# Kernel optimization log

Measured on AMD Instinct MI355X. Metric: run time of the kernel, lower is better.

Reference implementation:

```python
import jax, jax.numpy as jnp
import numpy as np

N_NODES, N_EDGES, B, K, D = 200000, 500000, 8192, 32, 128
E_DIM, E_EMB, N_CLASS = 128, 128, 60


def setup_inputs() -> dict:
    key = jax.random.key(0)
    ks = jax.random.split(key, 16)
    s = lambda k, shape, scale=0.05: jax.random.normal(k, shape, dtype=jnp.float32) * scale
    return {
        'memory_emb': s(ks[0], (N_NODES, D), 1.0),
        'edge_feat': s(ks[1], (N_EDGES, E_DIM), 1.0),
        'W_q': s(ks[2], (D, D)),
        'W_k': s(ks[3], (D, D)),
        'a': s(ks[4], (2 * D,)),
        'We_w': s(ks[5], (E_DIM, E_EMB)),
        'We_b': s(ks[6], (E_EMB,)),
        'Wuc': s(ks[7], (D + 2 * D + E_EMB, D)),
        'Wc1': s(ks[8], (D, 128)),
        'Wc2': s(ks[9], (128, N_CLASS)),
        'src_idxs': jax.random.randint(ks[10], (B,), 0, N_NODES),
        'dst_idxs': jax.random.randint(ks[11], (B,), 0, N_NODES),
        'edge_idxs': jax.random.randint(ks[12], (B,), 0, N_EDGES),
        'src_neighbors': jax.random.randint(ks[13], (B, K), 0, N_NODES),
        'dst_neighbors': jax.random.randint(ks[14], (B, K), 0, N_NODES),
    }


def reference(memory_emb, edge_feat, W_q, W_k, a, We_w, We_b, Wuc, Wc1, Wc2,
              src_idxs, dst_idxs, edge_idxs, src_neighbors, dst_neighbors):
    def attend(idxs, nbrs):
        self_emb = memory_emb[idxs]                      # [B, D] gather
        nb = memory_emb[nbrs]                            # [B, K, D] gather
        q = self_emb @ W_q                               # [B, D]
        k = jnp.einsum('bkd,de->bke', nb, W_k)           # [B, K, D]
        # GAT-style score: leaky_relu(a . [q || k])
        sq = q @ a[:D]                                   # [B]
        sk = jnp.einsum('bkd,d->bk', k, a[D:])           # [B, K]
        score = jax.nn.leaky_relu(sq[:, None] + sk, 0.2)
        attn = jax.nn.softmax(score, axis=-1)            # [B, K]
        agg = jnp.einsum('bk,bkd->bd', attn, k)          # [B, D]
        return self_emb, agg

    src_e, src_h = attend(src_idxs, src_neighbors)
    dst_e, dst_h = attend(dst_idxs, dst_neighbors)
    e = edge_feat[edge_idxs] @ We_w + We_b               # edge embedding [B, E_EMB]
    msg_src = jax.nn.relu(jnp.concatenate([src_e, src_h, dst_h, e], -1) @ Wuc)
    msg_dst = jax.nn.relu(jnp.concatenate([dst_e, dst_h, src_h, e], -1) @ Wuc)
    logits_src = jax.nn.relu(msg_src @ Wc1) @ Wc2
    logits_dst = jax.nn.relu(msg_dst @ Wc1) @ Wc2
    return jnp.stack([logits_src, logits_dst])           # [2, B, N_CLASS]
```

## Files before the change

kernel.cpp:

```cpp
#include <hip/hip_runtime.h>

#define D 128
#define KNBR 32
#define BATCH 8192
#define NCLASS 60
#define NB 16
#define NP 32

__global__ __launch_bounds__(256) void k_prep(
    const float* __restrict__ Wq, const float* __restrict__ Wk,
    const float* __restrict__ a, const float* __restrict__ Wew,
    const float* __restrict__ Web, const float* __restrict__ Wuc,
    float* __restrict__ wqa, float* __restrict__ wka,
    float* __restrict__ be, float* __restrict__ Wcomb2)
{
    __shared__ float sB[128][129];
    int blk = blockIdx.x, tid = threadIdx.x;
    if (blk == 0) {
        for (int t = tid; t < 128 * 128; t += 256) sB[t >> 7][t & 127] = Wq[t];
        __syncthreads();
        if (tid < 128) {
            float s = 0.f;
            for (int j = 0; j < D; ++j) s += sB[tid][j] * a[j];
            wqa[tid] = s;
        }
        __syncthreads();
        for (int t = tid; t < 128 * 128; t += 256) sB[t >> 7][t & 127] = Wk[t];
        __syncthreads();
        if (tid < 128) {
            float s = 0.f;
            for (int j = 0; j < D; ++j) s += sB[tid][j] * a[D + j];
            wka[tid] = s;
        }
    } else if (blk == 1) {
        if (tid < 128) {
            float acc = 0.f;
            for (int j = 0; j < D; ++j) acc += Web[j] * Wuc[(size_t)(384 + j) * D + tid];
            be[tid] = acc;
        }
    } else {
        int g  = (blk - 2) >> 4;
        int rb = ((blk - 2) & 15) * 8;
        const float* A = (g == 2) ? Wew : Wk;
        const float* B = Wuc + (size_t)(128 + g * 128) * D;
        for (int t = tid; t < 128 * 128; t += 256) sB[t >> 7][t & 127] = B[t];
        __syncthreads();
        int j = tid & 127, half = tid >> 7;
        float acc[4] = {0.f, 0.f, 0.f, 0.f};
        int r0 = rb + half * 4;
        for (int t = 0; t < 128; ++t) {
            float bv = sB[t][j];
            #pragma unroll
            for (int m = 0; m < 4; ++m)
                acc[m] = fmaf(A[(size_t)(r0 + m) * D + t], bv, acc[m]);
        }
        #pragma unroll
        for (int m = 0; m < 4; ++m)
            Wcomb2[(size_t)(g * 128 + r0 + m) * D + j] = acc[m];
    }
}

__global__ __launch_bounds__(256, 2) void k_fused(
    const float* __restrict__ mem, const float* __restrict__ edge_feat,
    const float* __restrict__ Wuc, const float* __restrict__ Wcomb2,
    const float* __restrict__ be,
    const float* __restrict__ wqa, const float* __restrict__ wka,
    const float* __restrict__ Wc1, const float* __restrict__ Wc2,
    const int* __restrict__ src_idxs, const int* __restrict__ dst_idxs,
    const int* __restrict__ edge_idxs,
    const int* __restrict__ src_nb, const int* __restrict__ dst_nb,
    float* __restrict__ out)
{
    __shared__ __align__(16) float s_self[NP * 132];
    __shared__ __align__(16) float s_nbsum[NP * 132];
    __shared__ __align__(16) float Ast[32 * 33];
    __shared__ __align__(16) float Ws[32 * 128];
    __shared__ __align__(16) float msgT[128 * 35];
    __shared__ int s_eidx[NB];

    int tid = threadIdx.x;
    int b0 = blockIdx.x * NB;
    int lane = tid & 31;
    int grp  = tid >> 5;

    if (tid < NB) s_eidx[tid] = edge_idxs[b0 + tid];

    float4 wq4 = ((const float4*)wqa)[lane];
    float4 wk4 = ((const float4*)wka)[lane];

    for (int it = 0; it < 4; ++it) {
        int p = it * 8 + grp;
        int side = p >> 4;
        int bb = b0 + (p & 15);
        int self_idx = (side ? dst_idxs : src_idxs)[bb];
        int nb_idx = (side ? dst_nb : src_nb)[(size_t)bb * KNBR + lane];

        float4 sv = ((const float4*)(mem + (size_t)self_idx * D))[lane];
        *(float4*)&s_self[p * 132 + lane * 4] = sv;
        float sp = sv.x * wq4.x + sv.y * wq4.y + sv.z * wq4.z + sv.w * wq4.w;
        #pragma unroll
        for (int m = 1; m <= 16; m <<= 1) sp += __shfl_xor(sp, m, 32);
        float sq = sp;

        float myscore = 0.f;
        #pragma unroll 4
        for (int k = 0; k < KNBR; ++k) {
            int ik = __shfl(nb_idx, k, 32);
            float4 v = ((const float4*)(mem + (size_t)ik * D))[lane];
            float pr = v.x * wk4.x + v.y * wk4.y + v.z * wk4.z + v.w * wk4.w;
            #pragma unroll
            for (int m = 1; m <= 16; m <<= 1) pr += __shfl_xor(pr, m, 32);
            if (k == lane) myscore = pr;
        }
        float x = sq + myscore;
        x = (x >= 0.f) ? x : 0.2f * x;
        float mx = x;
        #pragma unroll
        for (int m = 1; m <= 16; m <<= 1) mx = fmaxf(mx, __shfl_xor(mx, m, 32));
        float e = __expf(x - mx);
        float sum = e;
        #pragma unroll
        for (int m = 1; m <= 16; m <<= 1) sum += __shfl_xor(sum, m, 32);
        float attn = e / sum;

        float4 acc = make_float4(0.f, 0.f, 0.f, 0.f);
        #pragma unroll 4
        for (int k = 0; k < KNBR; ++k) {
            int ik = __shfl(nb_idx, k, 32);
            float ak = __shfl(attn, k, 32);
            float4 v = ((const float4*)(mem + (size_t)ik * D))[lane];
            acc.x = fmaf(ak, v.x, acc.x);
            acc.y = fmaf(ak, v.y, acc.y);
            acc.z = fmaf(ak, v.z, acc.z);
            acc.w = fmaf(ak, v.w, acc.w);
        }
        *(float4*)&s_nbsum[p * 132 + lane * 4] = acc;
    }
    __syncthreads();

    int tr = tid >> 4, tc = tid & 15;
    int lc = tid & 31, lr = tid >> 5;
    int wc = tid & 127, wk2 = tid >> 7;
    float accB[2][8];
    #pragma unroll
    for (int i = 0; i < 2; ++i)
        #pragma unroll
        for (int j = 0; j < 8; ++j) accB[i][j] = 0.f;

    for (int kt = 0; kt < 16; ++kt) {
        int seg = kt >> 2, off = (kt & 3) * 32;
        #pragma unroll
        for (int q = 0; q < 4; ++q) {
            int r = lr + 8 * q;
            float v;
            if (seg == 0)      v = s_self[r * 132 + off + lc];
            else if (seg == 1) v = s_nbsum[r * 132 + off + lc];
            else if (seg == 2) v = s_nbsum[(r ^ 16) * 132 + off + lc];
            else               v = edge_feat[(size_t)s_eidx[r & 15] * D + off + lc];
            Ast[lc * 33 + r] = v;
        }
        int krow0 = kt * 32;
        #pragma unroll
        for (int pp = 0; pp < 16; ++pp) {
            int kk = wk2 + 2 * pp;
            int gr = krow0 + kk;
            Ws[kk * 128 + wc] = (gr < 128) ? Wuc[(size_t)gr * D + wc]
                                           : Wcomb2[(size_t)(gr - 128) * D + wc];
        }
        __syncthreads();
        #pragma unroll 8
        for (int kk = 0; kk < 32; ++kk) {
            float a0 = Ast[kk * 33 + tr * 2];
            float a1 = Ast[kk * 33 + tr * 2 + 1];
            float4 w0 = *(const float4*)&Ws[kk * 128 + tc * 4];
            float4 w1 = *(const float4*)&Ws[kk * 128 + 64 + tc * 4];
            float wr[8] = {w0.x, w0.y, w0.z, w0.w, w1.x, w1.y, w1.z, w1.w};
            #pragma unroll
            for (int j = 0; j < 8; ++j) {
                accB[0][j] = fmaf(a0, wr[j], accB[0][j]);
                accB[1][j] = fmaf(a1, wr[j], accB[1][j]);
            }
        }
        __syncthreads();
    }
    {
        float4 bv0 = *(const float4*)&be[tc * 4];
        float4 bv1 = *(const float4*)&be[64 + tc * 4];
        float b8[8] = {bv0.x, bv0.y, bv0.z, bv0.w, bv1.x, bv1.y, bv1.z, bv1.w};
        #pragma unroll
        for (int i = 0; i < 2; ++i) {
            int r = tr * 2 + i;
            #pragma unroll
            for (int j = 0; j < 4; ++j) {
                msgT[(tc * 4 + j) * 35 + r]        = fmaxf(accB[i][j] + b8[j], 0.f);
                msgT[(64 + tc * 4 + j) * 35 + r]   = fmaxf(accB[i][j + 4] + b8[j + 4], 0.f);
            }
        }
    }
    __syncthreads();

    float accC[2][8];
    #pragma unroll
    for (int i = 0; i < 2; ++i)
        #pragma unroll
        for (int j = 0; j < 8; ++j) accC[i][j] = 0.f;

    for (int kt = 0; kt < 4; ++kt) {
        int off = kt * 32;
        #pragma unroll
        for (int pp = 0; pp < 16; ++pp) {
            int kk = wk2 + 2 * pp;
            Ws[kk * 128 + wc] = Wc1[(size_t)(off + kk) * D + wc];
        }
        __syncthreads();
        #pragma unroll 8
        for (int kk = 0; kk < 32; ++kk) {
            float a0 = msgT[(off + kk) * 35 + tr * 2];
            float a1 = msgT[(off + kk) * 35 + tr * 2 + 1];
            float4 w0 = *(const float4*)&Ws[kk * 128 + tc * 4];
            float4 w1 = *(const float4*)&Ws[kk * 128 + 64 + tc * 4];
            float wr[8] = {w0.x, w0.y, w0.z, w0.w, w1.x, w1.y, w1.z, w1.w};
            #pragma unroll
            for (int j = 0; j < 8; ++j) {
                accC[0][j] = fmaf(a0, wr[j], accC[0][j]);
                accC[1][j] = fmaf(a1, wr[j], accC[1][j]);
            }
        }
        __syncthreads();
    }
    #pragma unroll
    for (int i = 0; i < 2; ++i) {
        int r = tr * 2 + i;
        #pragma unroll
        for (int j = 0; j < 4; ++j) {
            msgT[(tc * 4 + j) * 35 + r]      = fmaxf(accC[i][j], 0.f);
            msgT[(64 + tc * 4 + j) * 35 + r] = fmaxf(accC[i][j + 4], 0.f);
        }
    }
    __syncthreads();

    int r2 = tid & 31;
    int cs = tid >> 5;
    float acc2[8];
    #pragma unroll
    for (int j = 0; j < 8; ++j) acc2[j] = 0.f;

    for (int kt = 0; kt < 4; ++kt) {
        int off = kt * 32;
        for (int t = tid; t < 32 * 64; t += 256) {
            int kk = t >> 6, c = t & 63;
            Ws[t] = (c < NCLASS) ? Wc2[(size_t)(off + kk) * NCLASS + c] : 0.f;
        }
        __syncthreads();
        #pragma unroll 4
        for (int kk = 0; kk < 32; ++kk) {
            float h = msgT[(off + kk) * 35 + r2];
            float4 w0 = *(const float4*)&Ws[kk * 64 + cs * 8];
            float4 w1 = *(const float4*)&Ws[kk * 64 + cs * 8 + 4];
            acc2[0] = fmaf(h, w0.x, acc2[0]);
            acc2[1] = fmaf(h, w0.y, acc2[1]);
            acc2[2] = fmaf(h, w0.z, acc2[2]);
            acc2[3] = fmaf(h, w0.w, acc2[3]);
            acc2[4] = fmaf(h, w1.x, acc2[4]);
            acc2[5] = fmaf(h, w1.y, acc2[5]);
            acc2[6] = fmaf(h, w1.z, acc2[6]);
            acc2[7] = fmaf(h, w1.w, acc2[7]);
        }
        __syncthreads();
    }
    {
        int side = r2 >> 4;
        int bb = b0 + (r2 & 15);
        size_t orow = ((size_t)side * BATCH + bb) * NCLASS;
        #pragma unroll
        for (int j = 0; j < 8; ++j) {
            int c = cs * 8 + j;
            if (c < NCLASS) out[orow + c] = acc2[j];
        }
    }
}

extern "C" void kernel_launch(void* const* d_in, const int* in_sizes, int n_in,
                              void* d_out, int out_size, void* d_ws, size_t ws_size,
                              hipStream_t stream) {
    const float* mem       = (const float*)d_in[0];
    const float* edge_feat = (const float*)d_in[1];
    const float* Wq        = (const float*)d_in[2];
    const float* Wk        = (const float*)d_in[3];
    const float* a         = (const float*)d_in[4];
    const float* Wew       = (const float*)d_in[5];
    const float* Web       = (const float*)d_in[6];
    const float* Wuc       = (const float*)d_in[7];
    const float* Wc1       = (const float*)d_in[8];
    const float* Wc2       = (const float*)d_in[9];
    const int* src_idxs    = (const int*)d_in[10];
    const int* dst_idxs    = (const int*)d_in[11];
    const int* edge_idxs   = (const int*)d_in[12];
    const int* src_nb      = (const int*)d_in[13];
    const int* dst_nb      = (const int*)d_in[14];
    float* out = (float*)d_out;

    float* ws = (float*)d_ws;
    float* Wcomb2 = ws;
    float* be     = ws + 49152;
    float* wqa    = ws + 49280;
    float* wka    = ws + 49408;

    k_prep<<<50, 256, 0, stream>>>(Wq, Wk, a, Wew, Web, Wuc, wqa, wka, be, Wcomb2);
    k_fused<<<BATCH / NB, 256, 0, stream>>>(mem, edge_feat, Wuc, Wcomb2, be,
                                            wqa, wka, Wc1, Wc2,
                                            src_idxs, dst_idxs, edge_idxs,
                                            src_nb, dst_nb, out);
}
```

Measured before the change: 550.5 us.

## Precompute per-node attention scores to avoid second neighbor gather

Adds a kernel that computes q- and k-score scalars for every node by streaming the embedding table once. The fused kernel then only reads a scalar per neighbor for the softmax, eliminating one of the two full-row neighbor gathers. Shared memory is reorganized (transposed neighbor sums, self rows re-read from global) to allow higher occupancy. It adds a full pass over all nodes regardless of batch usage.

```diff
diff --git a/kernel.cpp b/kernel.cpp
--- a/kernel.cpp
+++ b/kernel.cpp
@@ -60,22 +60,46 @@
     }
 }
 
-__global__ __launch_bounds__(256, 2) void k_fused(
+__global__ __launch_bounds__(256) void k_scores(
+    const float* __restrict__ mem,
+    const float* __restrict__ wqa, const float* __restrict__ wka,
+    float* __restrict__ nsq, float* __restrict__ nsk)
+{
+    int tid = threadIdx.x, lane = tid & 31, grp = tid >> 5;
+    int n0 = blockIdx.x * 64 + grp * 8;
+    float4 wq4 = ((const float4*)wqa)[lane];
+    float4 wk4 = ((const float4*)wka)[lane];
+    #pragma unroll
+    for (int i = 0; i < 8; ++i) {
+        int n = n0 + i;
+        float4 v = ((const float4*)(mem + (size_t)n * D))[lane];
+        float pq = v.x * wq4.x + v.y * wq4.y + v.z * wq4.z + v.w * wq4.w;
+        float pk = v.x * wk4.x + v.y * wk4.y + v.z * wk4.z + v.w * wk4.w;
+        #pragma unroll
+        for (int m = 1; m <= 16; m <<= 1) {
+            pq += __shfl_xor(pq, m, 32);
+            pk += __shfl_xor(pk, m, 32);
+        }
+        if (lane == 0) nsq[n] = pq;
+        if (lane == 1) nsk[n] = pk;
+    }
+}
+
+__global__ __launch_bounds__(256, 3) void k_fused(
     const float* __restrict__ mem, const float* __restrict__ edge_feat,
     const float* __restrict__ Wuc, const float* __restrict__ Wcomb2,
     const float* __restrict__ be,
-    const float* __restrict__ wqa, const float* __restrict__ wka,
+    const float* __restrict__ nsq, const float* __restrict__ nsk,
     const float* __restrict__ Wc1, const float* __restrict__ Wc2,
     const int* __restrict__ src_idxs, const int* __restrict__ dst_idxs,
     const int* __restrict__ edge_idxs,
     const int* __restrict__ src_nb, const int* __restrict__ dst_nb,
     float* __restrict__ out)
 {
-    __shared__ __align__(16) float s_self[NP * 132];
-    __shared__ __align__(16) float s_nbsum[NP * 132];
-    __shared__ __align__(16) float Ast[32 * 33];
     __shared__ __align__(16) float Ws[32 * 128];
-    __shared__ __align__(16) float msgT[128 * 35];
+    __shared__ __align__(16) float nbT[128 * 33];
+    __shared__ __align__(16) float uni[128 * 33];
+    __shared__ int s_sidx[NP];
     __shared__ int s_eidx[NB];
 
     int tid = threadIdx.x;
@@ -83,36 +107,17 @@
     int lane = tid & 31;
     int grp  = tid >> 5;
 
+    if (tid < NP) s_sidx[tid] = ((tid >> 4) ? dst_idxs : src_idxs)[b0 + (tid & 15)];
     if (tid < NB) s_eidx[tid] = edge_idxs[b0 + tid];
-
-    float4 wq4 = ((const float4*)wqa)[lane];
-    float4 wk4 = ((const float4*)wka)[lane];
 
     for (int it = 0; it < 4; ++it) {
         int p = it * 8 + grp;
         int side = p >> 4;
         int bb = b0 + (p & 15);
         int self_idx = (side ? dst_idxs : src_idxs)[bb];
-        int nb_idx = (side ? dst_nb : src_nb)[(size_t)bb * KNBR + lane];
-
-        float4 sv = ((const float4*)(mem + (size_t)self_idx * D))[lane];
-        *(float4*)&s_self[p * 132 + lane * 4] = sv;
-        float sp = sv.x * wq4.x + sv.y * wq4.y + sv.z * wq4.z + sv.w * wq4.w;
-        #pragma unroll
-        for (int m = 1; m <= 16; m <<= 1) sp += __shfl_xor(sp, m, 32);
-        float sq = sp;
-
-        float myscore = 0.f;
-        #pragma unroll 4
-        for (int k = 0; k < KNBR; ++k) {
-            int ik = __shfl(nb_idx, k, 32);
-            float4 v = ((const float4*)(mem + (size_t)ik * D))[lane];
-            float pr = v.x * wk4.x + v.y * wk4.y + v.z * wk4.z + v.w * wk4.w;
-            #pragma unroll
-            for (int m = 1; m <= 16; m <<= 1) pr += __shfl_xor(pr, m, 32);
-            if (k == lane) myscore = pr;
-        }
-        float x = sq + myscore;
+        int ik = (side ? dst_nb : src_nb)[(size_t)bb * KNBR + lane];
+
+        float x = nsq[self_idx] + nsk[ik];
         x = (x >= 0.f) ? x : 0.2f * x;
         float mx = x;
         #pragma unroll
@@ -124,17 +129,20 @@
         float attn = e / sum;
 
         float4 acc = make_float4(0.f, 0.f, 0.f, 0.f);
-        #pragma unroll 4
+        #pragma unroll 8
         for (int k = 0; k < KNBR; ++k) {
-            int ik = __shfl(nb_idx, k, 32);
+            int ikk  = __shfl(ik, k, 32);
             float ak = __shfl(attn, k, 32);
-            float4 v = ((const float4*)(mem + (size_t)ik * D))[lane];
+            float4 v = ((const float4*)(mem + (size_t)ikk * D))[lane];
             acc.x = fmaf(ak, v.x, acc.x);
             acc.y = fmaf(ak, v.y, acc.y);
             acc.z = fmaf(ak, v.z, acc.z);
             acc.w = fmaf(ak, v.w, acc.w);
         }
-        *(float4*)&s_nbsum[p * 132 + lane * 4] = acc;
+        nbT[(lane * 4 + 0) * 33 + p] = acc.x;
+        nbT[(lane * 4 + 1) * 33 + p] = acc.y;
+        nbT[(lane * 4 + 2) * 33 + p] = acc.z;
+        nbT[(lane * 4 + 3) * 33 + p] = acc.w;
     }
     __syncthreads();
 
@@ -147,25 +155,19 @@
         #pragma unroll
         for (int j = 0; j < 8; ++j) accB[i][j] = 0.f;
 
-    for (int kt = 0; kt < 16; ++kt) {
-        int seg = kt >> 2, off = (kt & 3) * 32;
+    float* Ast = uni;
+
+    for (int kt = 0; kt < 4; ++kt) {
+        int off = kt * 32;
         #pragma unroll
         for (int q = 0; q < 4; ++q) {
             int r = lr + 8 * q;
-            float v;
-            if (seg == 0)      v = s_self[r * 132 + off + lc];
-            else if (seg == 1) v = s_nbsum[r * 132 + off + lc];
-            else if (seg == 2) v = s_nbsum[(r ^ 16) * 132 + off + lc];
-            else               v = edge_feat[(size_t)s_eidx[r & 15] * D + off + lc];
-            Ast[lc * 33 + r] = v;
-        }
-        int krow0 = kt * 32;
+            Ast[lc * 33 + r] = mem[(size_t)s_sidx[r] * D + off + lc];
+        }
         #pragma unroll
         for (int pp = 0; pp < 16; ++pp) {
             int kk = wk2 + 2 * pp;
-            int gr = krow0 + kk;
-            Ws[kk * 128 + wc] = (gr < 128) ? Wuc[(size_t)gr * D + wc]
-                                           : Wcomb2[(size_t)(gr - 128) * D + wc];
+            Ws[kk * 128 + wc] = Wuc[(size_t)(off + kk) * D + wc];
         }
         __syncthreads();
         #pragma unroll 8
@@ -183,6 +185,62 @@
         }
         __syncthreads();
     }
+    for (int kt = 4; kt < 12; ++kt) {
+        int off = (kt & 3) * 32;
+        int gr0 = kt * 32 - 128;
+        #pragma unroll
+        for (int pp = 0; pp < 16; ++pp) {
+            int kk = wk2 + 2 * pp;
+            Ws[kk * 128 + wc] = Wcomb2[(size_t)(gr0 + kk) * D + wc];
+        }
+        __syncthreads();
+        int r0 = (kt < 8) ? (tr * 2) : ((tr * 2) ^ 16);
+        #pragma unroll 8
+        for (int kk = 0; kk < 32; ++kk) {
+            float a0 = nbT[(off + kk) * 33 + r0];
+            float a1 = nbT[(off + kk) * 33 + r0 + 1];
+            float4 w0 = *(const float4*)&Ws[kk * 128 + tc * 4];
+            float4 w1 = *(const float4*)&Ws[kk * 128 + 64 + tc * 4];
+            float wr[8] = {w0.x, w0.y, w0.z, w0.w, w1.x, w1.y, w1.z, w1.w};
+            #pragma unroll
+            for (int j = 0; j < 8; ++j) {
+                accB[0][j] = fmaf(a0, wr[j], accB[0][j]);
+                accB[1][j] = fmaf(a1, wr[j], accB[1][j]);
+            }
+        }
+        __syncthreads();
+    }
+    for (int kt = 12; kt < 16; ++kt) {
+        int off = (kt & 3) * 32;
+        int gr0 = kt * 32 - 128;
+        #pragma unroll
+        for (int q = 0; q < 4; ++q) {
+            int r = lr + 8 * q;
+            Ast[lc * 33 + r] = edge_feat[(size_t)s_eidx[r & 15] * D + off + lc];
+        }
+        #pragma unroll
+        for (int pp = 0; pp < 16; ++pp) {
+            int kk = wk2 + 2 * pp;
+            Ws[kk * 128 + wc] = Wcomb2[(size_t)(gr0 + kk) * D + wc];
+        }
+        __syncthreads();
+        #pragma unroll 8
+        for (int kk = 0; kk < 32; ++kk) {
+            float a0 = Ast[kk * 33 + tr * 2];
+            float a1 = Ast[kk * 33 + tr * 2 + 1];
+            float4 w0 = *(const float4*)&Ws[kk * 128 + tc * 4];
+            float4 w1 = *(const float4*)&Ws[kk * 128 + 64 + tc * 4];
+            float wr[8] = {w0.x, w0.y, w0.z, w0.w, w1.x, w1.y, w1.z, w1.w};
+            #pragma unroll
+            for (int j = 0; j < 8; ++j) {
+                accB[0][j] = fmaf(a0, wr[j], accB[0][j]);
+                accB[1][j] = fmaf(a1, wr[j], accB[1][j]);
+            }
+        }
+        __syncthreads();
+    }
+
+    float* msgT = uni;
     {
         float4 bv0 = *(const float4*)&be[tc * 4];
         float4 bv1 = *(const float4*)&be[64 + tc * 4];
@@ -192,8 +250,8 @@
             int r = tr * 2 + i;
             #pragma unroll
             for (int j = 0; j < 4; ++j) {
-                msgT[(tc * 4 + j) * 35 + r]        = fmaxf(accB[i][j] + b8[j], 0.f);
-                msgT[(64 + tc * 4 + j) * 35 + r]   = fmaxf(accB[i][j + 4] + b8[j + 4], 0.f);
+                msgT[(tc * 4 + j) * 33 + r]      = fmaxf(accB[i][j] + b8[j], 0.f);
+                msgT[(64 + tc * 4 + j) * 33 + r] = fmaxf(accB[i][j + 4] + b8[j + 4], 0.f);
             }
         }
     }
@@ -215,8 +273,8 @@
         __syncthreads();
         #pragma unroll 8
         for (int kk = 0; kk < 32; ++kk) {
-            float a0 = msgT[(off + kk) * 35 + tr * 2];
-            float a1 = msgT[(off + kk) * 35 + tr * 2 + 1];
+            float a0 = msgT[(off + kk) * 33 + tr * 2];
+            float a1 = msgT[(off + kk) * 33 + tr * 2 + 1];
             float4 w0 = *(const float4*)&Ws[kk * 128 + tc * 4];
             float4 w1 = *(const float4*)&Ws[kk * 128 + 64 + tc * 4];
             float wr[8] = {w0.x, w0.y, w0.z, w0.w, w1.x, w1.y, w1.z, w1.w};
@@ -233,8 +291,8 @@
         int r = tr * 2 + i;
         #pragma unroll
         for (int j = 0; j < 4; ++j) {
-            msgT[(tc * 4 + j) * 35 + r]      = fmaxf(accC[i][j], 0.f);
-            msgT[(64 + tc * 4 + j) * 35 + r] = fmaxf(accC[i][j + 4], 0.f);
+            msgT[(tc * 4 + j) * 33 + r]      = fmaxf(accC[i][j], 0.f);
+            msgT[(64 + tc * 4 + j) * 33 + r] = fmaxf(accC[i][j + 4], 0.f);
         }
     }
     __syncthreads();
@@ -254,7 +312,7 @@
         __syncthreads();
         #pragma unroll 4
         for (int kk = 0; kk < 32; ++kk) {
-            float h = msgT[(off + kk) * 35 + r2];
+            float h = msgT[(off + kk) * 33 + r2];
             float4 w0 = *(const float4*)&Ws[kk * 64 + cs * 8];
             float4 w1 = *(const float4*)&Ws[kk * 64 + cs * 8 + 4];
             acc2[0] = fmaf(h, w0.x, acc2[0]);
@@ -305,10 +363,13 @@
     float* be     = ws + 49152;
     float* wqa    = ws + 49280;
     float* wka    = ws + 49408;
+    float* nsq    = ws + 49536;
+    float* nsk    = ws + 249536;
 
     k_prep<<<50, 256, 0, stream>>>(Wq, Wk, a, Wew, Web, Wuc, wqa, wka, be, Wcomb2);
+    k_scores<<<200000 / 64, 256, 0, stream>>>(mem, wqa, wka, nsq, nsk);
     k_fused<<<BATCH / NB, 256, 0, stream>>>(mem, edge_feat, Wuc, Wcomb2, be,
-                                            wqa, wka, Wc1, Wc2,
+                                            nsq, nsk, Wc1, Wc2,
                                             src_idxs, dst_idxs, edge_idxs,
                                             src_nb, dst_nb, out);
 }
```

Measured after the change: 495.2 us. 10.1% less time.
